# Performance work log

Hardware: AMD Instinct MI355X
Metric: run time of the kernel (lower is better)

The kernel has to match this reference:

```python
import jax, jax.numpy as jnp
import numpy as np

B, H, W, C = 4, 64, 64, 256
C8 = C // 8

def setup_inputs() -> dict:
    key = jax.random.key(0)
    k1, k2, k3, k4 = jax.random.split(key, 4)
    # glorot-uniform-ish init for 1x1 conv kernels stored as [Cin, Cout]
    def glorot(k, cin, cout):
        lim = np.sqrt(6.0 / (cin + cout)).astype(np.float32)
        return jax.random.uniform(k, (cin, cout), jnp.float32, -lim, lim)
    return {
        "x": jax.random.normal(k1, (B, H, W, C), jnp.float32),
        "kernel_f": glorot(k2, C, C8),
        "kernel_g": glorot(k3, C, C8),
        "kernel_h": glorot(k4, C, C),
        "gamma": jnp.zeros((1,), jnp.float32),
    }

def reference(x, kernel_f, kernel_g, kernel_h, gamma):
    b, h, w, c = x.shape
    n = h * w
    xf = x.reshape(b, n, c)                       # [B, N, C]
    # 1x1 convs == per-position matmuls
    f = jnp.einsum('bnc,cd->bnd', xf, kernel_f)   # [B, N, C/8]
    g = jnp.einsum('bnc,cd->bnd', xf, kernel_g)   # [B, N, C/8]
    hh = jnp.einsum('bnc,cd->bnd', xf, kernel_h)  # [B, N, C]
    s = jnp.einsum('bnd,bmd->bnm', g, f)          # [B, N, N]
    beta = jax.nn.softmax(s, axis=-1)
    o = jnp.einsum('bnm,bmc->bnc', beta, hh)      # [B, N, C]
    o = o.reshape(b, h, w, c)
    return gamma * o + x
```

## Files before the change

kernel.cpp:

```cpp
#include <hip/hip_runtime.h>
#include <hip/hip_bf16.h>

typedef __bf16 bf16x8 __attribute__((ext_vector_type(8)));
typedef float f32x4 __attribute__((ext_vector_type(4)));
typedef float f32x16 __attribute__((ext_vector_type(16)));
typedef unsigned short u16;
typedef unsigned int u32;
typedef const __attribute__((address_space(1))) u32 gu32;
typedef __attribute__((address_space(3))) u32 lu32;

__device__ __forceinline__ u16 f2bf_rne(float f){
  union { float f; u32 u; } v; v.f = f;
  u32 r = v.u + 0x7fffu + ((v.u >> 16) & 1u);
  return (u16)(r >> 16);
}
__device__ __forceinline__ u32 pack_trunc(float a, float b){
  union { float f; u32 u; } x, y; x.f = a; y.f = b;
  return (x.u >> 16) | (y.u & 0xffff0000u);
}
__device__ __forceinline__ void stage16(const u16* g, u16* l){
  __builtin_amdgcn_global_load_lds((gu32*)g, (lu32*)l, 16, 0, 0);
}
#define BARRIER_LGKM() asm volatile("s_waitcnt lgkmcnt(0)\n\ts_barrier" ::: "memory")

__global__ __launch_bounds__(256) void prep_kernel(
    const float* __restrict__ Wf, const float* __restrict__ Wg,
    const float* __restrict__ Wh, u16* __restrict__ WcatT){
  __shared__ float tile[32][33];
  const int tx = threadIdx.x & 31, ty = threadIdx.x >> 5;
  const int k0 = blockIdx.x * 32, n0 = blockIdx.y * 32;
  #pragma unroll
  for (int i = 0; i < 4; ++i){
    int k = k0 + ty + i * 8, n = n0 + tx;
    float v;
    if (n < 256)      v = Wh[k * 256 + n];
    else if (n < 288) v = Wf[k * 32 + (n - 256)];
    else              v = Wg[k * 32 + (n - 288)];
    tile[ty + i * 8][tx] = v;
  }
  __syncthreads();
  #pragma unroll
  for (int i = 0; i < 4; ++i){
    int n = n0 + ty + i * 8, k = k0 + tx;
    WcatT[n * 256 + k] = f2bf_rne(tile[tx][ty + i * 8]);
  }
}

__global__ __launch_bounds__(512) void proj_kernel(
    const float* __restrict__ x, const u16* __restrict__ WcatT,
    u16* __restrict__ Qg, u16* __restrict__ Kg, u16* __restrict__ Vfrag)
{
  __shared__ __align__(16) u16 smem[256 * 72];
  u16 (*xb)[264] = (u16(*)[264])smem;
  u16 (*Vr)[72]  = (u16(*)[72])smem;

  const int tid = threadIdx.x;
  const int lane = tid & 63, wave = tid >> 6;
  const int L = lane & 15, quad = lane >> 4;
  const int rowgrp = wave >> 1, colhalf = wave & 1;
  const int n0 = blockIdx.x * 64;

  const float4* xsrc = (const float4*)(x + (size_t)n0 * 256);
  #pragma unroll
  for (int j = 0; j < 8; ++j){
    int idx = j * 512 + tid;
    int row = idx >> 6, col4 = idx & 63;
    float4 v = xsrc[idx];
    u32 p0 = (u32)f2bf_rne(v.x) | ((u32)f2bf_rne(v.y) << 16);
    u32 p1 = (u32)f2bf_rne(v.z) | ((u32)f2bf_rne(v.w) << 16);
    *(uint2*)&xb[row][col4 * 4] = make_uint2(p0, p1);
  }
  __syncthreads();

  f32x4 acc[10];
  #pragma unroll
  for (int cc = 0; cc < 10; ++cc) acc[cc] = (f32x4){0.f, 0.f, 0.f, 0.f};

  #pragma unroll
  for (int kk = 0; kk < 8; ++kk){
    bf16x8 a = *(const bf16x8*)&xb[rowgrp * 16 + L][kk * 32 + quad * 8];
    #pragma unroll
    for (int cc = 0; cc < 10; ++cc){
      int ccg = colhalf * 10 + cc;
      bf16x8 bfr = *(const bf16x8*)(WcatT + (size_t)(ccg * 16 + L) * 256 + kk * 32 + quad * 8);
      acc[cc] = __builtin_amdgcn_mfma_f32_16x16x32_bf16(a, bfr, acc[cc], 0, 0, 0);
    }
  }

  if (colhalf){
    #pragma unroll
    for (int cc = 6; cc < 10; ++cc){
      int ccg = 10 + cc;
      u16* dst = (ccg < 18) ? Kg : Qg;
      int c = (ccg & 1) * 16 + L;
      #pragma unroll
      for (int r = 0; r < 4; ++r){
        int row = n0 + rowgrp * 16 + quad * 4 + r;
        dst[(size_t)row * 32 + c] = f2bf_rne(acc[cc][r]);
      }
    }
  }

  __syncthreads();

  {
    const int cmax = colhalf ? 6 : 10;
    for (int cc = 0; cc < cmax; ++cc){
      int ccg = colhalf * 10 + cc;
      int c = ccg * 16 + L;
      #pragma unroll
      for (int r = 0; r < 4; ++r){
        int tn = rowgrp * 16 + quad * 4 + r;
        int p  = ((tn & 15) << 2) | (tn >> 4);
        Vr[c][p] = f2bf_rne(acc[cc][r]);
      }
    }
  }
  __syncthreads();

  u16* Vblk = Vfrag + (size_t)blockIdx.x * (256 * 64);
  #pragma unroll
  for (int i = 0; i < 4; ++i){
    int idx = i * 512 + tid;
    *(uint4*)(Vblk + (size_t)idx * 8) = *(const uint4*)&Vr[idx & 255][(idx >> 8) * 8];
  }
}

__global__ __launch_bounds__(512, 4) void flash_kernel(
    const u16* __restrict__ Qg, const u16* __restrict__ Kg, const u16* __restrict__ Vfrag,
    u16* __restrict__ Opart, float* __restrict__ Lpart)
{
  constexpr float LOG2E = 1.44269504088896340736f;
  constexpr float SH    = -92.33248261689366f;
  __shared__ __align__(16) u16 Plds[128][72];
  __shared__ __align__(16) u16 Vlds[2][8192];

  const int tid = threadIdx.x, lane = tid & 63, wave = tid >> 6;
  const int L = lane & 15, quad = lane >> 4;
  const int m32 = lane & 31, h32 = lane >> 5;
  const int qquad = wave >> 1, chalf2 = wave & 1;
  const int b = blockIdx.y >> 1, chalf = blockIdx.y & 1;
  const int split = blockIdx.z;
  const int qblk = blockIdx.x * 128;

  const u16* Qb = Qg + (size_t)(b * 4096) * 32;
  const u16* Kb = Kg + (size_t)(b * 4096) * 32;
  const u16* Vb = Vfrag + (size_t)b * (64 * 256 * 64);

  const int g0 = split * 16;

  {
    const u16* vt = Vb + (size_t)g0 * (256 * 64);
    #pragma unroll
    for (int i = 0; i < 2; ++i){
      int c = wave * 2 + i;
      int ph = c >> 1, c64 = c & 1;
      stage16(vt + (size_t)(ph * 256 + chalf * 128 + c64 * 64) * 8 + lane * 8,
              &Vlds[0][(ph * 128 + c64 * 64) * 8]);
    }
  }
  bf16x8 qa = *(const bf16x8*)(Qb + (size_t)(qblk + wave * 16 + L) * 32 + quad * 8);
  const u16* kp0 = Kb + (size_t)(g0 * 64 + L) * 32 + quad * 8;
  bf16x8 kc0 = *(const bf16x8*)(kp0);
  bf16x8 kc1 = *(const bf16x8*)(kp0 + 512);
  bf16x8 kc2 = *(const bf16x8*)(kp0 + 1024);
  bf16x8 kc3 = *(const bf16x8*)(kp0 + 1536);

  f32x16 acc[2];
  #pragma unroll
  for (int ct = 0; ct < 2; ++ct)
    #pragma unroll
    for (int i = 0; i < 16; ++i) acc[ct][i] = 0.f;
  float lsum[4] = {0.f, 0.f, 0.f, 0.f};
  const f32x4 zero = (f32x4){0.f, 0.f, 0.f, 0.f};

  for (int kt = 0; kt < 16; ++kt){
    const int g = g0 + kt;

    bf16x8 kn0, kn1, kn2, kn3;
    if (kt < 15){
      const u16* vt = Vb + (size_t)(g + 1) * (256 * 64);
      #pragma unroll
      for (int i = 0; i < 2; ++i){
        int c = wave * 2 + i;
        int ph = c >> 1, c64 = c & 1;
        stage16(vt + (size_t)(ph * 256 + chalf * 128 + c64 * 64) * 8 + lane * 8,
                &Vlds[(kt + 1) & 1][(ph * 128 + c64 * 64) * 8]);
      }
      const u16* kpn = Kb + (size_t)((g + 1) * 64 + L) * 32 + quad * 8;
      kn0 = *(const bf16x8*)(kpn);
      kn1 = *(const bf16x8*)(kpn + 512);
      kn2 = *(const bf16x8*)(kpn + 1024);
      kn3 = *(const bf16x8*)(kpn + 1536);
    }

    f32x4 s0 = __builtin_amdgcn_mfma_f32_16x16x32_bf16(qa, kc0, zero, 0, 0, 0);
    f32x4 s1 = __builtin_amdgcn_mfma_f32_16x16x32_bf16(qa, kc1, zero, 0, 0, 0);
    f32x4 s2 = __builtin_amdgcn_mfma_f32_16x16x32_bf16(qa, kc2, zero, 0, 0, 0);
    f32x4 s3 = __builtin_amdgcn_mfma_f32_16x16x32_bf16(qa, kc3, zero, 0, 0, 0);

    #pragma unroll
    for (int r = 0; r < 4; ++r){
      float p0 = exp2f(fmaf(s0[r], LOG2E, SH));
      float p1 = exp2f(fmaf(s1[r], LOG2E, SH));
      float p2 = exp2f(fmaf(s2[r], LOG2E, SH));
      float p3 = exp2f(fmaf(s3[r], LOG2E, SH));
      lsum[r] += (p0 + p1) + (p2 + p3);
      *(uint2*)&Plds[wave * 16 + quad * 4 + r][L * 4] =
          make_uint2(pack_trunc(p0, p1), pack_trunc(p2, p3));
    }

    BARRIER_LGKM();

    #pragma unroll
    for (int ks = 0; ks < 4; ++ks){
      bf16x8 af = *(const bf16x8*)&Plds[qquad * 32 + m32][ks * 16 + h32 * 8];
      const int vbase = ((ks * 2 + h32) * 128 + chalf2 * 64 + m32) * 8;
      #pragma unroll
      for (int ct = 0; ct < 2; ++ct){
        bf16x8 vf = *(const bf16x8*)&Vlds[kt & 1][vbase + ct * 32 * 8];
        acc[ct] = __builtin_amdgcn_mfma_f32_32x32x16_bf16(af, vf, acc[ct], 0, 0, 0);
      }
    }

    BARRIER_LGKM();

    if (kt < 15){ kc0 = kn0; kc1 = kn1; kc2 = kn2; kc3 = kn3; }
  }

  u16* Ob = Opart + ((size_t)split * 16384 + (size_t)b * 4096 + qblk) * 256;
  #pragma unroll
  for (int ct = 0; ct < 2; ++ct){
    #pragma unroll
    for (int rg = 0; rg < 16; ++rg){
      int row = qquad * 32 + (rg & 3) + 8 * (rg >> 2) + 4 * h32;
      int c = chalf * 128 + chalf2 * 64 + ct * 32 + m32;
      Ob[(size_t)row * 256 + c] = (u16)(__float_as_uint(acc[ct][rg]) >> 16);
    }
  }
  #pragma unroll
  for (int r = 0; r < 4; ++r){
    lsum[r] += __shfl_xor(lsum[r], 1);
    lsum[r] += __shfl_xor(lsum[r], 2);
    lsum[r] += __shfl_xor(lsum[r], 4);
    lsum[r] += __shfl_xor(lsum[r], 8);
  }
  if (chalf == 0 && L == 0){
    float* Lp = Lpart + split * 16384 + b * 4096 + qblk + wave * 16;
    #pragma unroll
    for (int r = 0; r < 4; ++r) Lp[quad * 4 + r] = lsum[r];
  }
}

__global__ __launch_bounds__(256) void combine_kernel(
    const float* __restrict__ x, const float* __restrict__ gamma,
    const u16* __restrict__ Opart, const float* __restrict__ Lpart,
    float* __restrict__ out)
{
  const int t = threadIdx.x;
  const int row = blockIdx.x * 8 + (t >> 5);
  const int c0 = (t & 31) * 8;
  const size_t base = (size_t)row * 256 + c0;
  float os[8];
  #pragma unroll
  for (int i = 0; i < 8; ++i) os[i] = 0.f;
  float ls = 0.f;
  #pragma unroll
  for (int s = 0; s < 4; ++s){
    ls += Lpart[s * 16384 + row];
    uint4 u = *(const uint4*)(Opart + (size_t)s * 16384 * 256 + base);
    os[0] += __uint_as_float(u.x << 16);
    os[1] += __uint_as_float(u.x & 0xffff0000u);
    os[2] += __uint_as_float(u.y << 16);
    os[3] += __uint_as_float(u.y & 0xffff0000u);
    os[4] += __uint_as_float(u.z << 16);
    os[5] += __uint_as_float(u.z & 0xffff0000u);
    os[6] += __uint_as_float(u.w << 16);
    os[7] += __uint_as_float(u.w & 0xffff0000u);
  }
  const float r = gamma[0] / ls;
  float4 x0 = *(const float4*)(x + base);
  float4 x1 = *(const float4*)(x + base + 4);
  float4 o0, o1;
  o0.x = os[0] * r + x0.x;  o0.y = os[1] * r + x0.y;
  o0.z = os[2] * r + x0.z;  o0.w = os[3] * r + x0.w;
  o1.x = os[4] * r + x1.x;  o1.y = os[5] * r + x1.y;
  o1.z = os[6] * r + x1.z;  o1.w = os[7] * r + x1.w;
  *(float4*)(out + base)     = o0;
  *(float4*)(out + base + 4) = o1;
}

extern "C" void kernel_launch(void* const* d_in, const int* in_sizes, int n_in,
                              void* d_out, int out_size, void* d_ws, size_t ws_size,
                              hipStream_t stream) {
  const float* x     = (const float*)d_in[0];
  const float* Wf    = (const float*)d_in[1];
  const float* Wg    = (const float*)d_in[2];
  const float* Wh    = (const float*)d_in[3];
  const float* gamma = (const float*)d_in[4];
  float* out = (float*)d_out;

  u16* p = (u16*)d_ws;
  u16* Qg    = p;  p += 16384 * 32;
  u16* Kg    = p;  p += 16384 * 32;
  u16* Vfrag = p;  p += 4 * 64 * 256 * 64;
  u16* WcatT = p;  p += 320 * 256;
  u16* Opart = p;  p += (size_t)4 * 16384 * 256;
  float* Lpart = (float*)p;

  prep_kernel<<<dim3(8, 10), 256, 0, stream>>>(Wf, Wg, Wh, WcatT);
  proj_kernel<<<256, 512, 0, stream>>>(x, WcatT, Qg, Kg, Vfrag);
  flash_kernel<<<dim3(32, 8, 4), 512, 0, stream>>>(Qg, Kg, Vfrag, Opart, Lpart);
  combine_kernel<<<2048, 256, 0, stream>>>(x, gamma, Opart, Lpart, out);
}
```

Baseline: 181.8 us.

## Cover all channels per flash block, fold log2e into Q, single-buffer V

Each flash block now covers all 256 output channels, with each wave computing four 32-wide tiles instead of two. This halves the grid and removes the duplicate QK^T and softmax work that was done once per channel half. The log2(e) scale moves into the Q projection, and the exp uses the raw exp2 intrinsic with a perm-based bf16 pack (still truncation, now via one perm). V staging becomes single-buffered and is issued only after the PV barrier. That costs the overlap of the V load with compute and raises accumulator register pressure.

```diff
diff --git a/kernel.cpp b/kernel.cpp
--- a/kernel.cpp
+++ b/kernel.cpp
@@ -14,9 +14,8 @@
   u32 r = v.u + 0x7fffu + ((v.u >> 16) & 1u);
   return (u16)(r >> 16);
 }
-__device__ __forceinline__ u32 pack_trunc(float a, float b){
-  union { float f; u32 u; } x, y; x.f = a; y.f = b;
-  return (x.u >> 16) | (y.u & 0xffff0000u);
+__device__ __forceinline__ u32 pack2(float a, float b){
+  return __builtin_amdgcn_perm(__float_as_uint(a), __float_as_uint(b), 0x03020706u);
 }
 __device__ __forceinline__ void stage16(const u16* g, u16* l){
   __builtin_amdgcn_global_load_lds((gu32*)g, (lu32*)l, 16, 0, 0);
@@ -92,11 +91,12 @@
     for (int cc = 6; cc < 10; ++cc){
       int ccg = 10 + cc;
       u16* dst = (ccg < 18) ? Kg : Qg;
+      float sc = (ccg < 18) ? 1.0f : 1.44269504088896f;
       int c = (ccg & 1) * 16 + L;
       #pragma unroll
       for (int r = 0; r < 4; ++r){
         int row = n0 + rowgrp * 16 + quad * 4 + r;
-        dst[(size_t)row * 32 + c] = f2bf_rne(acc[cc][r]);
+        dst[(size_t)row * 32 + c] = f2bf_rne(acc[cc][r] * sc);
       }
     }
   }
@@ -130,17 +130,15 @@
     const u16* __restrict__ Qg, const u16* __restrict__ Kg, const u16* __restrict__ Vfrag,
     u16* __restrict__ Opart, float* __restrict__ Lpart)
 {
-  constexpr float LOG2E = 1.44269504088896340736f;
-  constexpr float SH    = -92.33248261689366f;
+  constexpr float SH = -92.33248261689366f;
   __shared__ __align__(16) u16 Plds[128][72];
-  __shared__ __align__(16) u16 Vlds[2][8192];
+  __shared__ __align__(16) u16 Vlds[16384];
 
   const int tid = threadIdx.x, lane = tid & 63, wave = tid >> 6;
   const int L = lane & 15, quad = lane >> 4;
   const int m32 = lane & 31, h32 = lane >> 5;
-  const int qquad = wave >> 1, chalf2 = wave & 1;
-  const int b = blockIdx.y >> 1, chalf = blockIdx.y & 1;
-  const int split = blockIdx.z;
+  const int qquad = wave & 3, chalf = wave >> 2;
+  const int b = blockIdx.y, split = blockIdx.z;
   const int qblk = blockIdx.x * 128;
 
   const u16* Qb = Qg + (size_t)(b * 4096) * 32;
@@ -148,15 +146,12 @@
   const u16* Vb = Vfrag + (size_t)b * (64 * 256 * 64);
 
   const int g0 = split * 16;
-
   {
     const u16* vt = Vb + (size_t)g0 * (256 * 64);
     #pragma unroll
-    for (int i = 0; i < 2; ++i){
-      int c = wave * 2 + i;
-      int ph = c >> 1, c64 = c & 1;
-      stage16(vt + (size_t)(ph * 256 + chalf * 128 + c64 * 64) * 8 + lane * 8,
-              &Vlds[0][(ph * 128 + c64 * 64) * 8]);
+    for (int i = 0; i < 4; ++i){
+      int chunk = wave * 4 + i;
+      stage16(vt + chunk * 512 + lane * 8, &Vlds[chunk * 512]);
     }
   }
   bf16x8 qa = *(const bf16x8*)(Qb + (size_t)(qblk + wave * 16 + L) * 32 + quad * 8);
@@ -166,9 +161,9 @@
   bf16x8 kc2 = *(const bf16x8*)(kp0 + 1024);
   bf16x8 kc3 = *(const bf16x8*)(kp0 + 1536);
 
-  f32x16 acc[2];
-  #pragma unroll
-  for (int ct = 0; ct < 2; ++ct)
+  f32x16 acc[4];
+  #pragma unroll
+  for (int ct = 0; ct < 4; ++ct)
     #pragma unroll
     for (int i = 0; i < 16; ++i) acc[ct][i] = 0.f;
   float lsum[4] = {0.f, 0.f, 0.f, 0.f};
@@ -177,16 +172,26 @@
   for (int kt = 0; kt < 16; ++kt){
     const int g = g0 + kt;
 
+    f32x4 s0 = __builtin_amdgcn_mfma_f32_16x16x32_bf16(qa, kc0, zero, 0, 0, 0);
+    f32x4 s1 = __builtin_amdgcn_mfma_f32_16x16x32_bf16(qa, kc1, zero, 0, 0, 0);
+    f32x4 s2 = __builtin_amdgcn_mfma_f32_16x16x32_bf16(qa, kc2, zero, 0, 0, 0);
+    f32x4 s3 = __builtin_amdgcn_mfma_f32_16x16x32_bf16(qa, kc3, zero, 0, 0, 0);
+
+    #pragma unroll
+    for (int r = 0; r < 4; ++r){
+      float p0 = __builtin_amdgcn_exp2f(s0[r] + SH);
+      float p1 = __builtin_amdgcn_exp2f(s1[r] + SH);
+      float p2 = __builtin_amdgcn_exp2f(s2[r] + SH);
+      float p3 = __builtin_amdgcn_exp2f(s3[r] + SH);
+      lsum[r] += (p0 + p1) + (p2 + p3);
+      *(uint2*)&Plds[wave * 16 + quad * 4 + r][L * 4] =
+          make_uint2(pack2(p0, p1), pack2(p2, p3));
+    }
+
+    __syncthreads();
+
     bf16x8 kn0, kn1, kn2, kn3;
     if (kt < 15){
-      const u16* vt = Vb + (size_t)(g + 1) * (256 * 64);
-      #pragma unroll
-      for (int i = 0; i < 2; ++i){
-        int c = wave * 2 + i;
-        int ph = c >> 1, c64 = c & 1;
-        stage16(vt + (size_t)(ph * 256 + chalf * 128 + c64 * 64) * 8 + lane * 8,
-                &Vlds[(kt + 1) & 1][(ph * 128 + c64 * 64) * 8]);
-      }
       const u16* kpn = Kb + (size_t)((g + 1) * 64 + L) * 32 + quad * 8;
       kn0 = *(const bf16x8*)(kpn);
       kn1 = *(const bf16x8*)(kpn + 512);
@@ -194,47 +199,37 @@
       kn3 = *(const bf16x8*)(kpn + 1536);
     }
 
-    f32x4 s0 = __builtin_amdgcn_mfma_f32_16x16x32_bf16(qa, kc0, zero, 0, 0, 0);
-    f32x4 s1 = __builtin_amdgcn_mfma_f32_16x16x32_bf16(qa, kc1, zero, 0, 0, 0);
-    f32x4 s2 = __builtin_amdgcn_mfma_f32_16x16x32_bf16(qa, kc2, zero, 0, 0, 0);
-    f32x4 s3 = __builtin_amdgcn_mfma_f32_16x16x32_bf16(qa, kc3, zero, 0, 0, 0);
-
-    #pragma unroll
-    for (int r = 0; r < 4; ++r){
-      float p0 = exp2f(fmaf(s0[r], LOG2E, SH));
-      float p1 = exp2f(fmaf(s1[r], LOG2E, SH));
-      float p2 = exp2f(fmaf(s2[r], LOG2E, SH));
-      float p3 = exp2f(fmaf(s3[r], LOG2E, SH));
-      lsum[r] += (p0 + p1) + (p2 + p3);
-      *(uint2*)&Plds[wave * 16 + quad * 4 + r][L * 4] =
-          make_uint2(pack_trunc(p0, p1), pack_trunc(p2, p3));
-    }
-
-    BARRIER_LGKM();
-
     #pragma unroll
     for (int ks = 0; ks < 4; ++ks){
       bf16x8 af = *(const bf16x8*)&Plds[qquad * 32 + m32][ks * 16 + h32 * 8];
-      const int vbase = ((ks * 2 + h32) * 128 + chalf2 * 64 + m32) * 8;
+      const int vbase = ((ks * 2 + h32) * 256 + chalf * 128 + m32) * 8;
       #pragma unroll
-      for (int ct = 0; ct < 2; ++ct){
-        bf16x8 vf = *(const bf16x8*)&Vlds[kt & 1][vbase + ct * 32 * 8];
+      for (int ct = 0; ct < 4; ++ct){
+        bf16x8 vf = *(const bf16x8*)&Vlds[vbase + ct * 32 * 8];
         acc[ct] = __builtin_amdgcn_mfma_f32_32x32x16_bf16(af, vf, acc[ct], 0, 0, 0);
       }
     }
 
     BARRIER_LGKM();
 
-    if (kt < 15){ kc0 = kn0; kc1 = kn1; kc2 = kn2; kc3 = kn3; }
+    if (kt < 15){
+      const u16* vt = Vb + (size_t)(g + 1) * (256 * 64);
+      #pragma unroll
+      for (int i = 0; i < 4; ++i){
+        int chunk = wave * 4 + i;
+        stage16(vt + chunk * 512 + lane * 8, &Vlds[chunk * 512]);
+      }
+      kc0 = kn0; kc1 = kn1; kc2 = kn2; kc3 = kn3;
+    }
   }
 
   u16* Ob = Opart + ((size_t)split * 16384 + (size_t)b * 4096 + qblk) * 256;
   #pragma unroll
-  for (int ct = 0; ct < 2; ++ct){
+  for (int ct = 0; ct < 4; ++ct){
     #pragma unroll
     for (int rg = 0; rg < 16; ++rg){
       int row = qquad * 32 + (rg & 3) + 8 * (rg >> 2) + 4 * h32;
-      int c = chalf * 128 + chalf2 * 64 + ct * 32 + m32;
+      int c = chalf * 128 + ct * 32 + m32;
       Ob[(size_t)row * 256 + c] = (u16)(__float_as_uint(acc[ct][rg]) >> 16);
     }
   }
@@ -245,7 +240,7 @@
     lsum[r] += __shfl_xor(lsum[r], 4);
     lsum[r] += __shfl_xor(lsum[r], 8);
   }
-  if (chalf == 0 && L == 0){
+  if (L == 0){
     float* Lp = Lpart + split * 16384 + b * 4096 + qblk + wave * 16;
     #pragma unroll
     for (int r = 0; r < 4; ++r) Lp[quad * 4 + r] = lsum[r];
@@ -310,6 +305,6 @@
 
   prep_kernel<<<dim3(8, 10), 256, 0, stream>>>(Wf, Wg, Wh, WcatT);
   proj_kernel<<<256, 512, 0, stream>>>(x, WcatT, Qg, Kg, Vfrag);
-  flash_kernel<<<dim3(32, 8, 4), 512, 0, stream>>>(Qg, Kg, Vfrag, Opart, Lpart);
+  flash_kernel<<<dim3(32, 4, 4), 512, 0, stream>>>(Qg, Kg, Vfrag, Opart, Lpart);
   combine_kernel<<<2048, 256, 0, stream>>>(x, gamma, Opart, Lpart, out);
 }
```

After: 161.0 us. 1.13x faster.
